# Kernel tuning notes

Measured on AMD Instinct MI355X. Metric: run time of the kernel, lower is better.

The kernel has to match this reference:

```python
import jax, jax.numpy as jnp
import numpy as np

D_MODEL = 1024
NUM_HEADS = 16
HEAD_DIM = D_MODEL // NUM_HEADS
B, S = 4, 2048


def setup_inputs() -> dict:
    key = jax.random.key(0)
    ks = jax.random.split(key, 11)
    scale = 1.0 / np.sqrt(D_MODEL)
    return {
        "query": jax.random.normal(ks[0], (B, S, D_MODEL), jnp.float32),
        "key": jax.random.normal(ks[1], (B, S, D_MODEL), jnp.float32),
        "value": jax.random.normal(ks[2], (B, S, D_MODEL), jnp.float32),
        "Wq": jax.random.normal(ks[3], (D_MODEL, D_MODEL), jnp.float32) * scale,
        "bq": jnp.zeros((D_MODEL,), jnp.float32),
        "Wk": jax.random.normal(ks[4], (D_MODEL, D_MODEL), jnp.float32) * scale,
        "bk": jnp.zeros((D_MODEL,), jnp.float32),
        "Wv": jax.random.normal(ks[5], (D_MODEL, D_MODEL), jnp.float32) * scale,
        "bv": jnp.zeros((D_MODEL,), jnp.float32),
        "Wo": jax.random.normal(ks[6], (D_MODEL, D_MODEL), jnp.float32) * scale,
        "bo": jnp.zeros((D_MODEL,), jnp.float32),
    }


def reference(query, key, value, Wq, bq, Wk, bk, Wv, bv, Wo, bo):
    b = query.shape[0]
    # nn.Linear: x @ W.T + b; weights stored [out, in]
    def split_heads(x):
        return x.reshape(b, -1, NUM_HEADS, HEAD_DIM).transpose(0, 2, 1, 3)  # [b,h,s,d]
    q = split_heads(query @ Wq.T + bq)
    k = split_heads(key @ Wk.T + bk)
    v = split_heads(value @ Wv.T + bv)
    scores = jnp.einsum("bhqd,bhkd->bhqk", q, k) / np.sqrt(HEAD_DIM)
    weights = jax.nn.softmax(scores, axis=-1)
    out = jnp.einsum("bhqk,bhkd->bhqd", weights, v)
    out = out.transpose(0, 2, 1, 3).reshape(b, -1, D_MODEL)
    return out @ Wo.T + bo
```

## Files before the change

kernel.cpp:

```cpp
#include <hip/hip_runtime.h>

typedef __bf16 bf16;
typedef __bf16 bf16x4 __attribute__((ext_vector_type(4)));
typedef __bf16 bf16x8 __attribute__((ext_vector_type(8)));
typedef float f32x4 __attribute__((ext_vector_type(4)));

#define MFMA16(a, b, c) __builtin_amdgcn_mfma_f32_16x16x32_bf16((a), (b), (c), 0, 0, 0)

#define QSCALE 0.1803368808f

__device__ __forceinline__ void async_cp16(const bf16* g, bf16* l) {
    __builtin_amdgcn_global_load_lds((const __attribute__((address_space(1))) void*)g,
                                     (__attribute__((address_space(3))) void*)l, 16, 0, 0);
}

struct CvtArgs { const float* src[7]; bf16* dst[7]; };
__global__ void cvt_all(CvtArgs a) {
    int bx = blockIdx.x, t, off;
    if (bx < 12288) { t = bx >> 12;            off = bx & 4095; }
    else            { t = 3 + ((bx - 12288) >> 9); off = (bx - 12288) & 511; }
    size_t i = (size_t)off * 256 + threadIdx.x;
    const float4* p = (const float4*)(a.src[t] + i * 8);
    float4 x = p[0], y = p[1];
    bf16x8 o;
    o[0] = (bf16)x.x; o[1] = (bf16)x.y; o[2] = (bf16)x.z; o[3] = (bf16)x.w;
    o[4] = (bf16)y.x; o[5] = (bf16)y.y; o[6] = (bf16)y.z; o[7] = (bf16)y.w;
    *(bf16x8*)(a.dst[t] + i * 8) = o;
}

__device__ __forceinline__ void gemm_core(
    const bf16* __restrict__ A, const bf16* __restrict__ W,
    const float* __restrict__ bias, void* __restrict__ Cout,
    int mode, int m0, int n0)
{
    __shared__ bf16 As[128 * 64];
    __shared__ bf16 Bs[128 * 64];
    const int K = 1024;
    const int tid = threadIdx.x;
    const int lane = tid & 63, wave = tid >> 6;
    const int l15 = lane & 15, quad = lane >> 4, l7 = l15 & 7;
    const int wm = wave >> 1, wn = wave & 1;

    f32x4 acc[4][4] = {};

    const int rb = tid >> 3;
    const int cg8 = ((tid & 7) ^ (rb & 7)) * 8;
    const bf16* Ag = A + (size_t)(m0 + rb) * K + cg8;
    const bf16* Wg = W + (size_t)(n0 + rb) * K + cg8;
    bf16* Al = As + tid * 8;
    bf16* Bl = Bs + tid * 8;

    for (int k0 = 0; k0 < K; k0 += 64) {
        __syncthreads();
#pragma unroll
        for (int j = 0; j < 4; ++j) {
            async_cp16(Ag + k0 + (size_t)(j * 32) * K, Al + j * 2048);
            async_cp16(Wg + k0 + (size_t)(j * 32) * K, Bl + j * 2048);
        }
        __syncthreads();

#pragma unroll
        for (int ks = 0; ks < 2; ++ks) {
            bf16x8 af[4], bfr[4];
#pragma unroll
            for (int t = 0; t < 4; ++t) {
                const int sw = ((ks * 4 + quad) ^ l7) * 8;
                af[t]  = *(const bf16x8*)(As + (wm * 64 + t * 16 + l15) * 64 + sw);
                bfr[t] = *(const bf16x8*)(Bs + (wn * 64 + t * 16 + l15) * 64 + sw);
            }
#pragma unroll
            for (int mt = 0; mt < 4; ++mt)
#pragma unroll
                for (int nt = 0; nt < 4; ++nt)
                    acc[mt][nt] = MFMA16(af[mt], bfr[nt], acc[mt][nt]);
        }
    }

#pragma unroll
    for (int mt = 0; mt < 4; ++mt) {
#pragma unroll
        for (int nt = 0; nt < 4; ++nt) {
            int col = n0 + wn * 64 + nt * 16 + l15;
            float bcol = (mode == 2) ? 0.0f : bias[col];
#pragma unroll
            for (int r = 0; r < 4; ++r) {
                int row = m0 + wm * 64 + mt * 16 + quad * 4 + r;
                float val = acc[mt][nt][r];
                if (mode == 2) {
                    val += bias[row];
                    int bb = col >> 11, s = col & 2047;
                    int u = s & 31;
                    int sp = (s & ~31) | (((u >> 2) & 3) * 8 + (u >> 4) * 4 + (u & 3));
                    ((bf16*)Cout)[((size_t)(bb * 1024 + row) << 11) + sp] = (bf16)val;
                } else if (mode == 3) {
                    ((float*)Cout)[(size_t)row * 1024 + col] = val + bcol;
                } else {
                    val += bcol;
                    if (mode == 0) val *= QSCALE;
                    int bb = row >> 11, s = row & 2047, hh = col >> 6, d = col & 63;
                    ((bf16*)Cout)[(((size_t)(bb * 16 + hh) * 2048 + s) << 6) + d] = (bf16)val;
                }
            }
        }
    }
}

struct QkvArgs {
    const bf16* A[3];
    const bf16* W[3];
    const float* bias[3];
    bf16* out[3];
};

__global__ __launch_bounds__(256) void qkv_gemm(QkvArgs t) {
    int z = blockIdx.y;
    int bid = blockIdx.x;
    int lo = bid & 7, mid = (bid >> 3) & 7, hi = bid >> 6;
    int m0, n0;
    if (z < 2) { m0 = (lo + hi * 8) * 128; n0 = mid * 128; }
    else       { m0 = mid * 128;           n0 = (lo + hi * 8) * 128; }
    gemm_core(t.A[z], t.W[z], t.bias[z], t.out[z], z, m0, n0);
}

__global__ __launch_bounds__(256) void oproj_gemm(
    const bf16* __restrict__ A, const bf16* __restrict__ W,
    const float* __restrict__ bias, float* __restrict__ Cout) {
    gemm_core(A, W, bias, Cout, 3, blockIdx.x * 128, blockIdx.y * 128);
}

__global__ __launch_bounds__(256, 4) void attn_kernel(
    const bf16* __restrict__ Qh, const bf16* __restrict__ Kh,
    const bf16* __restrict__ Vtg, bf16* __restrict__ AO)
{
    __shared__ bf16 Kl[64 * 64];
    __shared__ bf16 Vl[64 * 64];

    const int tid = threadIdx.x;
    const int lane = tid & 63, wave = tid >> 6;
    const int l15 = lane & 15, quad = lane >> 4, l7 = l15 & 7;
    const int g = blockIdx.x & 63, qi = blockIdx.x >> 6;
    const int h = g & 15, b = g >> 4;
    const size_t base = (size_t)(b * 16 + h) << 17;
    const int q0 = qi * 128 + wave * 32;

    bf16x8 qf[2][2];
#pragma unroll
    for (int qt = 0; qt < 2; ++qt)
#pragma unroll
        for (int ks = 0; ks < 2; ++ks)
            qf[qt][ks] = *(const bf16x8*)(Qh + base + (q0 + qt * 16 + l15) * 64 + ks * 32 + quad * 8);

    f32x4 o[4][2] = {};
    float ls[2] = {};

    const int sr = tid >> 3;
    const int sc0 = ((tid & 7) ^ (sr & 7)) * 8;
    const int sr2 = sr + 32;

    for (int kt = 0; kt < 2048; kt += 64) {
        __syncthreads();
        async_cp16(Kh + base + (size_t)(kt + sr) * 64 + sc0, Kl + tid * 8);
        async_cp16(Kh + base + (size_t)(kt + sr2) * 64 + sc0, Kl + (tid + 256) * 8);
        async_cp16(Vtg + base + (size_t)sr * 2048 + kt + sc0, Vl + tid * 8);
        async_cp16(Vtg + base + (size_t)sr2 * 2048 + kt + sc0, Vl + (tid + 256) * 8);
        __syncthreads();

        bf16x8 kb[2][4];
#pragma unroll
        for (int ks = 0; ks < 2; ++ks)
#pragma unroll
            for (int ktile = 0; ktile < 4; ++ktile)
                kb[ks][ktile] = *(const bf16x8*)(Kl + (ktile * 16 + l15) * 64 + (((ks * 4 + quad) ^ l7) * 8));

        bf16x8 pf[2][2];
#pragma unroll
        for (int qt = 0; qt < 2; ++qt) {
            f32x4 sc[4] = {};
#pragma unroll
            for (int ks = 0; ks < 2; ++ks)
#pragma unroll
                for (int ktile = 0; ktile < 4; ++ktile)
                    sc[ktile] = MFMA16(kb[ks][ktile], qf[qt][ks], sc[ktile]);
            float sum = 0.0f;
#pragma unroll
            for (int kc = 0; kc < 2; ++kc) {
                bf16x8 pk;
#pragma unroll
                for (int t = 0; t < 2; ++t)
#pragma unroll
                    for (int r = 0; r < 4; ++r) {
                        float p = __builtin_amdgcn_exp2f(sc[kc * 2 + t][r]);
                        sum += p;
                        pk[t * 4 + r] = (bf16)p;
                    }
                pf[qt][kc] = pk;
            }
            ls[qt] += sum;
        }

        bf16x8 va[4][2];
#pragma unroll
        for (int dt = 0; dt < 4; ++dt)
#pragma unroll
            for (int kc = 0; kc < 2; ++kc)
                va[dt][kc] = *(const bf16x8*)(Vl + (dt * 16 + l15) * 64 + (((kc * 4 + quad) ^ l7) * 8));

#pragma unroll
        for (int dt = 0; dt < 4; ++dt)
#pragma unroll
            for (int qt = 0; qt < 2; ++qt)
#pragma unroll
                for (int kc = 0; kc < 2; ++kc)
                    o[dt][qt] = MFMA16(va[dt][kc], pf[qt][kc], o[dt][qt]);
    }

#pragma unroll
    for (int qt = 0; qt < 2; ++qt) {
        float l = ls[qt];
        l += __shfl_xor(l, 16, 64);
        l += __shfl_xor(l, 32, 64);
        float inv = 1.0f / l;
        size_t rb = ((size_t)(b * 2048 + q0 + qt * 16 + l15)) * 1024 + h * 64;
#pragma unroll
        for (int dt = 0; dt < 4; ++dt) {
            bf16x4 ov = {(bf16)(o[dt][qt][0] * inv), (bf16)(o[dt][qt][1] * inv),
                         (bf16)(o[dt][qt][2] * inv), (bf16)(o[dt][qt][3] * inv)};
            *(bf16x4*)(AO + rb + dt * 16 + quad * 4) = ov;
        }
    }
}

extern "C" void kernel_launch(void* const* d_in, const int* in_sizes, int n_in,
                              void* d_out, int out_size, void* d_ws, size_t ws_size,
                              hipStream_t stream) {
    const float* q  = (const float*)d_in[0];
    const float* k  = (const float*)d_in[1];
    const float* v  = (const float*)d_in[2];
    const float* Wq = (const float*)d_in[3];
    const float* bq = (const float*)d_in[4];
    const float* Wk = (const float*)d_in[5];
    const float* bk = (const float*)d_in[6];
    const float* Wv = (const float*)d_in[7];
    const float* bv = (const float*)d_in[8];
    const float* Wo = (const float*)d_in[9];
    const float* bo = (const float*)d_in[10];
    float* out = (float*)d_out;

    const size_t NX = (size_t)8192 * 1024;
    const size_t NW = (size_t)1024 * 1024;
    bf16* ws  = (bf16*)d_ws;
    bf16* Xq  = ws;
    bf16* Xk  = Xq + NX;
    bf16* Xv  = Xk + NX;
    bf16* Wqb = Xv + NX;
    bf16* Wkb = Wqb + NW;
    bf16* Wvb = Wkb + NW;
    bf16* Wob = Wvb + NW;
    bf16* Qh  = Wob + NW;
    bf16* Kh  = Qh + NX;
    bf16* Vt  = Kh + NX;
    bf16* AO  = Xq;

    CvtArgs ca;
    ca.src[0] = q;  ca.dst[0] = Xq;
    ca.src[1] = k;  ca.dst[1] = Xk;
    ca.src[2] = v;  ca.dst[2] = Xv;
    ca.src[3] = Wq; ca.dst[3] = Wqb;
    ca.src[4] = Wk; ca.dst[4] = Wkb;
    ca.src[5] = Wv; ca.dst[5] = Wvb;
    ca.src[6] = Wo; ca.dst[6] = Wob;
    cvt_all<<<14336, 256, 0, stream>>>(ca);

    QkvArgs t;
    t.A[0] = Xq;  t.W[0] = Wqb; t.bias[0] = bq; t.out[0] = Qh;
    t.A[1] = Xk;  t.W[1] = Wkb; t.bias[1] = bk; t.out[1] = Kh;
    t.A[2] = Wvb; t.W[2] = Xv;  t.bias[2] = bv; t.out[2] = Vt;
    qkv_gemm<<<dim3(512, 3), dim3(256, 1, 1), 0, stream>>>(t);

    attn_kernel<<<1024, 256, 0, stream>>>(Qh, Kh, Vt, AO);

    oproj_gemm<<<dim3(64, 8), dim3(256, 1, 1), 0, stream>>>(AO, Wob, bo, out);
}
```

Baseline: 340.5 us.

## Use 256x256 double-buffered 8-wave GEMM tile for QKV projection

Replaces the 128x128 QKV GEMM with a 256x256 tile computed by 512 threads. It double-buffers LDS with async global-to-LDS loads, interleaves the staging with MFMA phases using barriers and setprio, and remaps blocks in an XCD-aware order. The aim is more operand reuse, fewer blocks, and load latency hidden behind compute. The cost is 128KB of LDS per block, which limits occupancy, plus more barriers. Only 384 blocks are launched, so the tail effect across CUs may be uneven.

```diff
diff --git a/kernel.cpp b/kernel.cpp
--- a/kernel.cpp
+++ b/kernel.cpp
@@ -28,6 +28,155 @@
     *(bf16x8*)(a.dst[t] + i * 8) = o;
 }
 
+__device__ __forceinline__ void c_write(
+    float val, const float* __restrict__ bias, void* __restrict__ Cout,
+    int mode, int row, int col)
+{
+    if (mode == 2) {
+        val += bias[row];
+        int bb = col >> 11, s = col & 2047;
+        int u = s & 31;
+        int sp = (s & ~31) | (((u >> 2) & 3) * 8 + (u >> 4) * 4 + (u & 3));
+        ((bf16*)Cout)[((size_t)(bb * 1024 + row) << 11) + sp] = (bf16)val;
+    } else if (mode == 3) {
+        ((float*)Cout)[(size_t)row * 1024 + col] = val + bias[col];
+    } else {
+        val += bias[col];
+        if (mode == 0) val *= QSCALE;
+        int bb = row >> 11, s = row & 2047, hh = col >> 6, d = col & 63;
+        ((bf16*)Cout)[(((size_t)(bb * 16 + hh) * 2048 + s) << 6) + d] = (bf16)val;
+    }
+}
+
+__device__ __forceinline__ void gemm256(
+    const bf16* __restrict__ A, const bf16* __restrict__ W,
+    const float* __restrict__ bias, void* __restrict__ Cout,
+    int mode, int m0, int n0)
+{
+    __shared__ bf16 A0s[256 * 64], B0s[256 * 64];
+    __shared__ bf16 A1s[256 * 64], B1s[256 * 64];
+    const int K = 1024;
+    const int tid = threadIdx.x;
+    const int lane = tid & 63, wave = tid >> 6;
+    const int l15 = lane & 15, quad = lane >> 4, l7 = l15 & 7;
+    const int wm = wave >> 2, wn = wave & 3;
+
+    f32x4 acc[8][4] = {};
+
+    const int rb = tid >> 3;
+    const int cg8 = ((tid & 7) ^ (rb & 7)) * 8;
+    const bf16* Ag = A + (size_t)(m0 + rb) * K + cg8;
+    const bf16* Wg = W + (size_t)(n0 + rb) * K + cg8;
+
+    auto stageA = [&](bf16* An, int kn) {
+#pragma unroll
+        for (int j = 0; j < 4; ++j)
+            async_cp16(Ag + kn + (size_t)(j * 64) * K, An + j * 4096 + tid * 8);
+    };
+    auto stageB = [&](bf16* Bn, int kn) {
+#pragma unroll
+        for (int j = 0; j < 4; ++j)
+            async_cp16(Wg + kn + (size_t)(j * 64) * K, Bn + j * 4096 + tid * 8);
+    };
+
+    const int sw0 = (quad ^ l7) * 8;
+    const int sw1 = ((4 + quad) ^ l7) * 8;
+
+    auto ktile = [&](const bf16* Ac, const bf16* Bc, bf16* An, bf16* Bn,
+                     int kn, bool st) {
+        bf16x8 bf[4], af[4];
+#pragma unroll
+        for (int nt = 0; nt < 4; ++nt)
+            bf[nt] = *(const bf16x8*)(Bc + (wn * 64 + nt * 16 + l15) * 64 + sw0);
+#pragma unroll
+        for (int mt = 0; mt < 4; ++mt)
+            af[mt] = *(const bf16x8*)(Ac + (wm * 128 + mt * 16 + l15) * 64 + sw0);
+        if (st) stageA(An, kn);
+        __builtin_amdgcn_s_barrier();
+        asm volatile("s_waitcnt lgkmcnt(0)" ::: "memory");
+        __builtin_amdgcn_sched_barrier(0);
+        __builtin_amdgcn_s_setprio(1);
+#pragma unroll
+        for (int mt = 0; mt < 4; ++mt)
+#pragma unroll
+            for (int nt = 0; nt < 4; ++nt)
+                acc[mt][nt] = MFMA16(af[mt], bf[nt], acc[mt][nt]);
+        __builtin_amdgcn_s_setprio(0);
+        __builtin_amdgcn_s_barrier();
+#pragma unroll
+        for (int mt = 0; mt < 4; ++mt)
+            af[mt] = *(const bf16x8*)(Ac + (wm * 128 + (mt + 4) * 16 + l15) * 64 + sw0);
+        if (st) stageB(Bn, kn);
+        __builtin_amdgcn_s_barrier();
+        asm volatile("s_waitcnt lgkmcnt(0)" ::: "memory");
+        __builtin_amdgcn_sched_barrier(0);
+        __builtin_amdgcn_s_setprio(1);
+#pragma unroll
+        for (int mt = 0; mt < 4; ++mt)
+#pragma unroll
+            for (int nt = 0; nt < 4; ++nt)
+                acc[mt + 4][nt] = MFMA16(af[mt], bf[nt], acc[mt + 4][nt]);
+        __builtin_amdgcn_s_setprio(0);
+        __builtin_amdgcn_s_barrier();
+#pragma unroll
+        for (int nt = 0; nt < 4; ++nt)
+            bf[nt] = *(const bf16x8*)(Bc + (wn * 64 + nt * 16 + l15) * 64 + sw1);
+#pragma unroll
+        for (int mt = 0; mt < 4; ++mt)
+            af[mt] = *(const bf16x8*)(Ac + (wm * 128 + mt * 16 + l15) * 64 + sw1);
+        __builtin_amdgcn_s_barrier();
+        asm volatile("s_waitcnt lgkmcnt(0)" ::: "memory");
+        __builtin_amdgcn_sched_barrier(0);
+        __builtin_amdgcn_s_setprio(1);
+#pragma unroll
+        for (int mt = 0; mt < 4; ++mt)
+#pragma unroll
+            for (int nt = 0; nt < 4; ++nt)
+                acc[mt][nt] = MFMA16(af[mt], bf[nt], acc[mt][nt]);
+        __builtin_amdgcn_s_setprio(0);
+        __builtin_amdgcn_s_barrier();
+#pragma unroll
+        for (int mt = 0; mt < 4; ++mt)
+            af[mt] = *(const bf16x8*)(Ac + (wm * 128 + (mt + 4) * 16 + l15) * 64 + sw1);
+        __builtin_amdgcn_s_barrier();
+        asm volatile("s_waitcnt lgkmcnt(0)" ::: "memory");
+        __builtin_amdgcn_sched_barrier(0);
+        __builtin_amdgcn_s_setprio(1);
+#pragma unroll
+        for (int mt = 0; mt < 4; ++mt)
+#pragma unroll
+            for (int nt = 0; nt < 4; ++nt)
+                acc[mt + 4][nt] = MFMA16(af[mt], bf[nt], acc[mt + 4][nt]);
+        __builtin_amdgcn_s_setprio(0);
+        if (st) asm volatile("s_waitcnt vmcnt(0)" ::: "memory");
+        __builtin_amdgcn_s_barrier();
+    };
+
+    stageA(A0s, 0); stageB(B0s, 0);
+    asm volatile("s_waitcnt vmcnt(0)" ::: "memory");
+    __builtin_amdgcn_s_barrier();
+
+    for (int p = 0; p < 7; ++p) {
+        ktile(A0s, B0s, A1s, B1s, (2 * p + 1) * 64, true);
+        ktile(A1s, B1s, A0s, B0s, (2 * p + 2) * 64, true);
+    }
+    ktile(A0s, B0s, A1s, B1s, 960, true);
+    ktile(A1s, B1s, A0s, B0s, 0, false);
+
+#pragma unroll
+    for (int mt = 0; mt < 8; ++mt) {
+#pragma unroll
+        for (int nt = 0; nt < 4; ++nt) {
+            int col = n0 + wn * 64 + nt * 16 + l15;
+#pragma unroll
+            for (int r = 0; r < 4; ++r) {
+                int row = m0 + wm * 128 + mt * 16 + quad * 4 + r;
+                c_write(acc[mt][nt][r], bias, Cout, mode, row, col);
+            }
+        }
+    }
+}
+
 __device__ __forceinline__ void gemm_core(
     const bf16* __restrict__ A, const bf16* __restrict__ W,
     const float* __restrict__ bias, void* __restrict__ Cout,
@@ -77,32 +226,16 @@
     }
 
 #pragma unroll
-    for (int mt = 0; mt < 4; ++mt) {
+    for (int mt = 0; mt < 4; ++mt)
 #pragma unroll
         for (int nt = 0; nt < 4; ++nt) {
             int col = n0 + wn * 64 + nt * 16 + l15;
-            float bcol = (mode == 2) ? 0.0f : bias[col];
 #pragma unroll
             for (int r = 0; r < 4; ++r) {
                 int row = m0 + wm * 64 + mt * 16 + quad * 4 + r;
-                float val = acc[mt][nt][r];
-                if (mode == 2) {
-                    val += bias[row];
-                    int bb = col >> 11, s = col & 2047;
-                    int u = s & 31;
-                    int sp = (s & ~31) | (((u >> 2) & 3) * 8 + (u >> 4) * 4 + (u & 3));
-                    ((bf16*)Cout)[((size_t)(bb * 1024 + row) << 11) + sp] = (bf16)val;
-                } else if (mode == 3) {
-                    ((float*)Cout)[(size_t)row * 1024 + col] = val + bcol;
-                } else {
-                    val += bcol;
-                    if (mode == 0) val *= QSCALE;
-                    int bb = row >> 11, s = row & 2047, hh = col >> 6, d = col & 63;
-                    ((bf16*)Cout)[(((size_t)(bb * 16 + hh) * 2048 + s) << 6) + d] = (bf16)val;
-                }
+                c_write(acc[mt][nt][r], bias, Cout, mode, row, col);
             }
         }
-    }
 }
 
 struct QkvArgs {
@@ -112,14 +245,14 @@
     bf16* out[3];
 };
 
-__global__ __launch_bounds__(256) void qkv_gemm(QkvArgs t) {
-    int z = blockIdx.y;
+__global__ __launch_bounds__(512, 2) void qkv_gemm(QkvArgs t) {
     int bid = blockIdx.x;
-    int lo = bid & 7, mid = (bid >> 3) & 7, hi = bid >> 6;
+    int idx = (bid & 7) * 48 + (bid >> 3);
+    int z = idx >> 7, r = idx & 127;
     int m0, n0;
-    if (z < 2) { m0 = (lo + hi * 8) * 128; n0 = mid * 128; }
-    else       { m0 = mid * 128;           n0 = (lo + hi * 8) * 128; }
-    gemm_core(t.A[z], t.W[z], t.bias[z], t.out[z], z, m0, n0);
+    if (z < 2) { m0 = (r >> 2) * 256; n0 = (r & 3) * 256; }
+    else       { m0 = (r & 3) * 256;  n0 = (r >> 2) * 256; }
+    gemm256(t.A[z], t.W[z], t.bias[z], t.out[z], z, m0, n0);
 }
 
 __global__ __launch_bounds__(256) void oproj_gemm(
@@ -275,7 +408,7 @@
     t.A[0] = Xq;  t.W[0] = Wqb; t.bias[0] = bq; t.out[0] = Qh;
     t.A[1] = Xk;  t.W[1] = Wkb; t.bias[1] = bk; t.out[1] = Kh;
     t.A[2] = Wvb; t.W[2] = Xv;  t.bias[2] = bv; t.out[2] = Vt;
-    qkv_gemm<<<dim3(512, 3), dim3(256, 1, 1), 0, stream>>>(t);
+    qkv_gemm<<<384, 512, 0, stream>>>(t);
 
     attn_kernel<<<1024, 256, 0, stream>>>(Qh, Kh, Vt, AO);
 
```

Result: slower. 352.9 us (+3.6%).

## Fuse all four stages into one persistent cooperative kernel with grid syncs

Applied to the files above, without the earlier changes.

Replaces the four separate launches (convert, QKV GEMM, attention, output projection) with a single cooperative kernel of 1024 blocks that loops over work units and uses grid-wide syncs between stages. The aim is to remove launch gaps and tail effects between kernels. In exchange, the GEMM stage now runs under an occupancy limit of 4 blocks per CU with a shared 32KB LDS buffer, and the 1536 QKV tiles are spread unevenly over 1024 blocks. Only 512 blocks take part in the output projection. If the cooperative launch fails, the code falls back to the original four launches.

```diff
diff --git a/kernel.cpp b/kernel.cpp
--- a/kernel.cpp
+++ b/kernel.cpp
@@ -1,4 +1,7 @@
 #include <hip/hip_runtime.h>
+#include <hip/hip_cooperative_groups.h>
+
+namespace cg = cooperative_groups;
 
 typedef __bf16 bf16;
 typedef __bf16 bf16x4 __attribute__((ext_vector_type(4)));
@@ -15,9 +18,9 @@
 }
 
 struct CvtArgs { const float* src[7]; bf16* dst[7]; };
-__global__ void cvt_all(CvtArgs a) {
-    int bx = blockIdx.x, t, off;
-    if (bx < 12288) { t = bx >> 12;            off = bx & 4095; }
+__device__ __forceinline__ void cvt_unit(const CvtArgs& a, int bx) {
+    int t, off;
+    if (bx < 12288) { t = bx >> 12;                off = bx & 4095; }
     else            { t = 3 + ((bx - 12288) >> 9); off = (bx - 12288) & 511; }
     size_t i = (size_t)off * 256 + threadIdx.x;
     const float4* p = (const float4*)(a.src[t] + i * 8);
@@ -28,13 +31,11 @@
     *(bf16x8*)(a.dst[t] + i * 8) = o;
 }
 
-__device__ __forceinline__ void gemm_core(
+__device__ __forceinline__ void gemm_tile(
     const bf16* __restrict__ A, const bf16* __restrict__ W,
     const float* __restrict__ bias, void* __restrict__ Cout,
-    int mode, int m0, int n0)
+    int mode, int m0, int n0, bf16* As, bf16* Bs)
 {
-    __shared__ bf16 As[128 * 64];
-    __shared__ bf16 Bs[128 * 64];
     const int K = 1024;
     const int tid = threadIdx.x;
     const int lane = tid & 63, wave = tid >> 6;
@@ -103,42 +104,18 @@
             }
         }
     }
-}
-
-struct QkvArgs {
-    const bf16* A[3];
-    const bf16* W[3];
-    const float* bias[3];
-    bf16* out[3];
-};
-
-__global__ __launch_bounds__(256) void qkv_gemm(QkvArgs t) {
-    int z = blockIdx.y;
-    int bid = blockIdx.x;
-    int lo = bid & 7, mid = (bid >> 3) & 7, hi = bid >> 6;
-    int m0, n0;
-    if (z < 2) { m0 = (lo + hi * 8) * 128; n0 = mid * 128; }
-    else       { m0 = mid * 128;           n0 = (lo + hi * 8) * 128; }
-    gemm_core(t.A[z], t.W[z], t.bias[z], t.out[z], z, m0, n0);
-}
-
-__global__ __launch_bounds__(256) void oproj_gemm(
-    const bf16* __restrict__ A, const bf16* __restrict__ W,
-    const float* __restrict__ bias, float* __restrict__ Cout) {
-    gemm_core(A, W, bias, Cout, 3, blockIdx.x * 128, blockIdx.y * 128);
-}
-
-__global__ __launch_bounds__(256, 4) void attn_kernel(
+    __syncthreads();
+}
+
+__device__ __forceinline__ void attn_tile(
     const bf16* __restrict__ Qh, const bf16* __restrict__ Kh,
-    const bf16* __restrict__ Vtg, bf16* __restrict__ AO)
+    const bf16* __restrict__ Vtg, bf16* __restrict__ AO,
+    int bid, bf16* Kl, bf16* Vl)
 {
-    __shared__ bf16 Kl[64 * 64];
-    __shared__ bf16 Vl[64 * 64];
-
     const int tid = threadIdx.x;
     const int lane = tid & 63, wave = tid >> 6;
     const int l15 = lane & 15, quad = lane >> 4, l7 = l15 & 7;
-    const int g = blockIdx.x & 63, qi = blockIdx.x >> 6;
+    const int g = bid & 63, qi = bid >> 6;
     const int h = g & 15, b = g >> 4;
     const size_t base = (size_t)(b * 16 + h) << 17;
     const int q0 = qi * 128 + wave * 32;
@@ -228,6 +205,77 @@
             *(bf16x4*)(AO + rb + dt * 16 + quad * 4) = ov;
         }
     }
+    __syncthreads();
+}
+
+struct QkvArgs {
+    const bf16* A[3];
+    const bf16* W[3];
+    const float* bias[3];
+    bf16* out[3];
+};
+
+struct FusedArgs {
+    CvtArgs cvt;
+    QkvArgs qkv;
+    const bf16* Qh; const bf16* Kh; const bf16* Vt; bf16* AO;
+    const bf16* Wob; const float* bo; float* out;
+};
+
+__global__ __launch_bounds__(256, 4) void fused_mha(FusedArgs a) {
+    __shared__ __align__(16) bf16 smem[16384];
+    cg::grid_group grid = cg::this_grid();
+
+    for (int u = blockIdx.x; u < 14336; u += 1024) cvt_unit(a.cvt, u);
+    grid.sync();
+
+    for (int v = blockIdx.x; v < 1536; v += 1024) {
+        int z = v >> 9, bid = v & 511;
+        int lo = bid & 7, mid = (bid >> 3) & 7, hi = bid >> 6;
+        int m0, n0;
+        if (z < 2) { m0 = (lo + hi * 8) * 128; n0 = mid * 128; }
+        else       { m0 = mid * 128;           n0 = (lo + hi * 8) * 128; }
+        gemm_tile(a.qkv.A[z], a.qkv.W[z], a.qkv.bias[z], a.qkv.out[z], z,
+                  m0, n0, smem, smem + 8192);
+    }
+    grid.sync();
+
+    attn_tile(a.Qh, a.Kh, a.Vt, a.AO, blockIdx.x, smem, smem + 4096);
+    grid.sync();
+
+    if (blockIdx.x < 512) {
+        int v = blockIdx.x;
+        gemm_tile(a.AO, a.Wob, a.bo, a.out, 3, (v & 63) * 128, (v >> 6) * 128,
+                  smem, smem + 8192);
+    }
+}
+
+__global__ void cvt_all(CvtArgs a) { cvt_unit(a, blockIdx.x); }
+
+__global__ __launch_bounds__(256) void qkv_gemm(QkvArgs t) {
+    __shared__ __align__(16) bf16 smem[16384];
+    int z = blockIdx.y;
+    int bid = blockIdx.x;
+    int lo = bid & 7, mid = (bid >> 3) & 7, hi = bid >> 6;
+    int m0, n0;
+    if (z < 2) { m0 = (lo + hi * 8) * 128; n0 = mid * 128; }
+    else       { m0 = mid * 128;           n0 = (lo + hi * 8) * 128; }
+    gemm_tile(t.A[z], t.W[z], t.bias[z], t.out[z], z, m0, n0, smem, smem + 8192);
+}
+
+__global__ __launch_bounds__(256) void oproj_gemm(
+    const bf16* __restrict__ A, const bf16* __restrict__ W,
+    const float* __restrict__ bias, float* __restrict__ Cout) {
+    __shared__ __align__(16) bf16 smem[16384];
+    gemm_tile(A, W, bias, Cout, 3, blockIdx.x * 128, blockIdx.y * 128,
+              smem, smem + 8192);
+}
+
+__global__ __launch_bounds__(256, 4) void attn_kernel(
+    const bf16* __restrict__ Qh, const bf16* __restrict__ Kh,
+    const bf16* __restrict__ Vtg, bf16* __restrict__ AO) {
+    __shared__ __align__(16) bf16 smem[8192];
+    attn_tile(Qh, Kh, Vtg, AO, blockIdx.x, smem, smem + 4096);
 }
 
 extern "C" void kernel_launch(void* const* d_in, const int* in_sizes, int n_in,
@@ -261,23 +309,28 @@
     bf16* Vt  = Kh + NX;
     bf16* AO  = Xq;
 
-    CvtArgs ca;
-    ca.src[0] = q;  ca.dst[0] = Xq;
-    ca.src[1] = k;  ca.dst[1] = Xk;
-    ca.src[2] = v;  ca.dst[2] = Xv;
-    ca.src[3] = Wq; ca.dst[3] = Wqb;
-    ca.src[4] = Wk; ca.dst[4] = Wkb;
-    ca.src[5] = Wv; ca.dst[5] = Wvb;
-    ca.src[6] = Wo; ca.dst[6] = Wob;
-    cvt_all<<<14336, 256, 0, stream>>>(ca);
-
-    QkvArgs t;
-    t.A[0] = Xq;  t.W[0] = Wqb; t.bias[0] = bq; t.out[0] = Qh;
-    t.A[1] = Xk;  t.W[1] = Wkb; t.bias[1] = bk; t.out[1] = Kh;
-    t.A[2] = Wvb; t.W[2] = Xv;  t.bias[2] = bv; t.out[2] = Vt;
-    qkv_gemm<<<dim3(512, 3), dim3(256, 1, 1), 0, stream>>>(t);
-
-    attn_kernel<<<1024, 256, 0, stream>>>(Qh, Kh, Vt, AO);
-
-    oproj_gemm<<<dim3(64, 8), dim3(256, 1, 1), 0, stream>>>(AO, Wob, bo, out);
-}
+    FusedArgs fa;
+    fa.cvt.src[0] = q;  fa.cvt.dst[0] = Xq;
+    fa.cvt.src[1] = k;  fa.cvt.dst[1] = Xk;
+    fa.cvt.src[2] = v;  fa.cvt.dst[2] = Xv;
+    fa.cvt.src[3] = Wq; fa.cvt.dst[3] = Wqb;
+    fa.cvt.src[4] = Wk; fa.cvt.dst[4] = Wkb;
+    fa.cvt.src[5] = Wv; fa.cvt.dst[5] = Wvb;
+    fa.cvt.src[6] = Wo; fa.cvt.dst[6] = Wob;
+    fa.qkv.A[0] = Xq;  fa.qkv.W[0] = Wqb; fa.qkv.bias[0] = bq; fa.qkv.out[0] = Qh;
+    fa.qkv.A[1] = Xk;  fa.qkv.W[1] = Wkb; fa.qkv.bias[1] = bk; fa.qkv.out[1] = Kh;
+    fa.qkv.A[2] = Wvb; fa.qkv.W[2] = Xv;  fa.qkv.bias[2] = bv; fa.qkv.out[2] = Vt;
+    fa.Qh = Qh; fa.Kh = Kh; fa.Vt = Vt; fa.AO = AO;
+    fa.Wob = Wob; fa.bo = bo; fa.out = out;
+
+    void* kargs[] = {(void*)&fa};
+    hipError_t err = hipLaunchCooperativeKernel((const void*)fused_mha,
+                                                dim3(1024), dim3(256),
+                                                kargs, 0, stream);
+    if (err != hipSuccess) {
+        cvt_all<<<14336, 256, 0, stream>>>(fa.cvt);
+        qkv_gemm<<<dim3(512, 3), dim3(256, 1, 1), 0, stream>>>(fa.qkv);
+        attn_kernel<<<1024, 256, 0, stream>>>(Qh, Kh, Vt, AO);
+        oproj_gemm<<<dim3(64, 8), dim3(256, 1, 1), 0, stream>>>(AO, Wob, bo, out);
+    }
+}
```

Result: slower. 762.2 us (+123.9%).
